# Kernel optimization log

Measured on AMD Instinct MI355X. Metric: run time of the kernel, lower is better.

Reference implementation:

```python
import jax, jax.numpy as jnp
import numpy as np

D_MODEL = 1024
NUM_HEADS = 16
D_K = D_MODEL // NUM_HEADS
SIM_THRESH = 0.7


def setup_inputs() -> dict:
    key = jax.random.key(0)
    ks = jax.random.split(key, 7)
    bs, seq = 2, 2048
    scale = 1.0 / np.sqrt(D_MODEL)
    x = jax.random.normal(ks[0], (bs, seq, D_MODEL), dtype=jnp.float32)
    Wq = jax.random.normal(ks[1], (D_MODEL, D_MODEL), dtype=jnp.float32) * scale
    Wk = jax.random.normal(ks[2], (D_MODEL, D_MODEL), dtype=jnp.float32) * scale
    Wv = jax.random.normal(ks[3], (D_MODEL, D_MODEL), dtype=jnp.float32) * scale
    bq = jax.random.normal(ks[4], (D_MODEL,), dtype=jnp.float32) * scale
    bk = jax.random.normal(ks[5], (D_MODEL,), dtype=jnp.float32) * scale
    bv = jax.random.normal(ks[6], (D_MODEL,), dtype=jnp.float32) * scale
    return {"x": x, "Wq": Wq, "bq": bq, "Wk": Wk, "bk": bk, "Wv": Wv, "bv": bv}


def reference(x, Wq, bq, Wk, bk, Wv, bv):
    bs, seq, d_model = x.shape
    # dynamic structural mask: cosine similarity > 0.7, shared across heads
    norm_x = x / jnp.maximum(jnp.linalg.norm(x, axis=-1, keepdims=True), 1e-12)
    sim = jnp.einsum('bsd,btd->bst', norm_x, norm_x)          # [B,S,S]
    mask = (sim > SIM_THRESH)[:, None, :, :]                  # [B,1,S,S]

    def proj(W, b):
        y = x @ W.T + b                                        # [B,S,D]
        return y.reshape(bs, seq, NUM_HEADS, D_K).transpose(0, 2, 1, 3)  # [B,H,S,dk]

    q = proj(Wq, bq)
    k = proj(Wk, bk)
    v = proj(Wv, bv)

    scores = jnp.einsum('bhsd,bhtd->bhst', q, k) / jnp.sqrt(jnp.float32(D_K))
    scores = jnp.where(mask, scores, -jnp.inf)
    attn = jax.nn.softmax(scores, axis=-1)                     # diag always unmasked
    return jnp.einsum('bhst,bhtd->bhsd', attn, v)              # [B,H,S,dk]
```

## Files before the change

kernel.cpp:

```cpp
#include <hip/hip_runtime.h>
#include <stdint.h>
#include <math.h>

#define D_MODEL 1024
#define NUM_HEADS 16
#define D_K 64
#define SEQ 2048
#define BATCH 2
#define SIM_THRESH 0.7f

#define TS 128
#define BK 32
#define NIT (D_MODEL / BK)

#define NROWS (BATCH * SEQ)
#define VP_BLOCKS ((NROWS / TS) * (D_MODEL / TS))
#define SIM_ROWB (SEQ / TS)
#define SIM_TRI (SIM_ROWB * (SIM_ROWB + 1) / 2)
#define SIM_BLOCKS (SIM_TRI * BATCH)
#define GRID (VP_BLOCKS + SIM_BLOCKS)

#define TILE_SH (TS * BK)

typedef __attribute__((ext_vector_type(8))) short bf16x8;
typedef __attribute__((ext_vector_type(4))) float f32x4;

static __device__ __forceinline__ unsigned short f2bf(float f) {
    unsigned int u = __float_as_uint(f);
    unsigned int r = (u + 0x7FFF + ((u >> 16) & 1)) >> 16;
    return (unsigned short)r;
}
static __device__ __forceinline__ float bf2f(unsigned short u) {
    return __uint_as_float(((unsigned int)u) << 16);
}

__global__ __launch_bounds__(256) void k_prep(const float* __restrict__ x,
                                              const float* __restrict__ Wv,
                                              unsigned short* __restrict__ xn,
                                              unsigned short* __restrict__ Wvb,
                                              float* __restrict__ norms,
                                              int* __restrict__ cnt) {
    int bid = blockIdx.x, tid = threadIdx.x;
    if (bid < NROWS) {
        const float4* xr = (const float4*)(x + (size_t)bid * D_MODEL);
        float4 vv = xr[tid];
        float ss = vv.x * vv.x + vv.y * vv.y + vv.z * vv.z + vv.w * vv.w;
        for (int off = 32; off > 0; off >>= 1) ss += __shfl_down(ss, off, 64);
        __shared__ float wsum[4];
        int lane = tid & 63, wv = tid >> 6;
        if (lane == 0) wsum[wv] = ss;
        __syncthreads();
        float nrm = sqrtf(wsum[0] + wsum[1] + wsum[2] + wsum[3]);
        float inv = 1.0f / fmaxf(nrm, 1e-12f);
        ushort4 o;
        o.x = f2bf(vv.x * inv); o.y = f2bf(vv.y * inv);
        o.z = f2bf(vv.z * inv); o.w = f2bf(vv.w * inv);
        *(ushort4*)(xn + (size_t)bid * D_MODEL + tid * 4) = o;
        if (tid == 0) { norms[bid] = nrm; cnt[bid] = 0; }
    } else {
        size_t i = (size_t)(bid - NROWS) * 256 + tid;
        float4 w = ((const float4*)Wv)[i];
        ushort4 o;
        o.x = f2bf(w.x); o.y = f2bf(w.y); o.z = f2bf(w.z); o.w = f2bf(w.w);
        *(ushort4*)(Wvb + i * 4) = o;
    }
}

static __device__ __forceinline__ void stage128x32(const unsigned short* __restrict__ gsrc,
                                                   int kk, short* ldsDst, int tid) {
#pragma unroll
    for (int i = 0; i < 2; ++i) {
        int c   = i * 256 + tid;
        int row = c >> 2;
        int ch  = c & 3;
        const unsigned short* ga = gsrc + (size_t)row * D_MODEL + kk + ch * 8;
        __builtin_amdgcn_global_load_lds(
            (const __attribute__((address_space(1))) unsigned int*)ga,
            (__attribute__((address_space(3))) unsigned int*)(ldsDst + c * 8),
            16, 0, 0);
    }
}

__global__ __launch_bounds__(256) void k_main(const unsigned short* __restrict__ xn,
                                              const unsigned short* __restrict__ Wvb,
                                              const float* __restrict__ bv,
                                              const float* __restrict__ norms,
                                              int* __restrict__ cnt,
                                              float* __restrict__ out) {
    __shared__ short As[2 * TILE_SH];
    __shared__ short Bs[2 * TILE_SH];
    int bid = blockIdx.x;
    int tid = threadIdx.x;
    int lane = tid & 63, wave = tid >> 6;
    int wm = wave & 1, wn = wave >> 1;
    int lrow = lane & 15, quad = lane >> 4;

    const unsigned short* Asrc;
    const unsigned short* Bsrc;
    int rowBase, colBase;
    bool isV;
    int b = 0, bi = 0, bj = 0;
    if (bid < VP_BLOCKS) {
        isV = true;
        rowBase = (bid >> 3) * TS;
        colBase = (bid & 7) * TS;
        Asrc = xn + (size_t)rowBase * D_MODEL;
        Bsrc = Wvb + (size_t)colBase * D_MODEL;
    } else {
        isV = false;
        int sidx = bid - VP_BLOCKS;
        b = (sidx >= SIM_TRI) ? 1 : 0;
        int r = sidx - b * SIM_TRI;
        bi = 0;
        while (r >= SIM_ROWB - bi) { r -= SIM_ROWB - bi; ++bi; }
        bj = bi + r;
        rowBase = bi * TS;
        colBase = bj * TS;
        const unsigned short* base = xn + (size_t)b * SEQ * D_MODEL;
        Asrc = base + (size_t)rowBase * D_MODEL;
        Bsrc = base + (size_t)colBase * D_MODEL;
    }

    int aoff[4], boff[4];
#pragma unroll
    for (int i = 0; i < 4; ++i) {
        aoff[i] = (wm * 64 + i * 16 + lrow) * BK + quad * 8;
        boff[i] = (wn * 64 + i * 16 + lrow) * BK + quad * 8;
    }
    f32x4 acc[4][4] = {};

    stage128x32(Asrc, 0, As, tid);
    stage128x32(Bsrc, 0, Bs, tid);
    __syncthreads();
    for (int it = 0; it < NIT; ++it) {
        int cur = it & 1, nxt = cur ^ 1;
        if (it + 1 < NIT) {
            stage128x32(Asrc, (it + 1) * BK, As + nxt * TILE_SH, tid);
            stage128x32(Bsrc, (it + 1) * BK, Bs + nxt * TILE_SH, tid);
        }
        const short* Ac = As + cur * TILE_SH;
        const short* Bc = Bs + cur * TILE_SH;
        bf16x8 av[4], bvv[4];
#pragma unroll
        for (int i = 0; i < 4; ++i) av[i]  = *(const bf16x8*)(Ac + aoff[i]);
#pragma unroll
        for (int i = 0; i < 4; ++i) bvv[i] = *(const bf16x8*)(Bc + boff[i]);
#pragma unroll
        for (int mt = 0; mt < 4; ++mt)
#pragma unroll
            for (int nt = 0; nt < 4; ++nt)
                acc[mt][nt] = __builtin_amdgcn_mfma_f32_16x16x32_bf16(av[mt], bvv[nt], acc[mt][nt], 0, 0, 0);
        __syncthreads();
    }

    if (isV) {
#pragma unroll
        for (int nt = 0; nt < 4; ++nt) {
            int n = colBase + wn * 64 + nt * 16 + lrow;
            float bn = bv[n];
            int h = n >> 6, j = n & 63;
#pragma unroll
            for (int mt = 0; mt < 4; ++mt) {
#pragma unroll
                for (int r = 0; r < 4; ++r) {
                    int m = rowBase + wm * 64 + mt * 16 + quad * 4 + r;
                    float val = acc[mt][nt][r] * norms[m] + bn;
                    int bb = m >> 11, s = m & (SEQ - 1);
                    out[(((size_t)(bb * NUM_HEADS + h)) * SEQ + s) * D_K + j] = val;
                }
            }
        }
    } else {
        int* cb = cnt + b * SEQ;
        bool diag = (bi == bj);
#pragma unroll
        for (int nt = 0; nt < 4; ++nt) {
            int n = colBase + wn * 64 + nt * 16 + lrow;
#pragma unroll
            for (int mt = 0; mt < 4; ++mt) {
#pragma unroll
                for (int r = 0; r < 4; ++r) {
                    int m = rowBase + wm * 64 + mt * 16 + quad * 4 + r;
                    if (acc[mt][nt][r] > SIM_THRESH) {
                        atomicAdd(&cb[m], 1);
                        if (!diag) atomicAdd(&cb[n], 1);
                    }
                }
            }
        }
    }
}

__global__ __launch_bounds__(256) void k_fix(
    const float* __restrict__ x,
    const float* __restrict__ Wq, const float* __restrict__ bq,
    const float* __restrict__ Wk, const float* __restrict__ bk,
    const float* __restrict__ Wv, const float* __restrict__ bv,
    const unsigned short* __restrict__ xn,
    const int* __restrict__ cnt,
    float* __restrict__ out)
{
    int tid = threadIdx.x;
    int rowBase = blockIdx.x * 256;

    __shared__ int list[256];
    __shared__ int nlist;
    if (tid == 0) nlist = 0;
    __syncthreads();
    int grow = rowBase + tid;
    if (cnt[grow] != 1) { int p = atomicAdd(&nlist, 1); list[p] = grow; }
    __syncthreads();
    int nfix = nlist;
    if (nfix == 0) return;

    __shared__ uint8_t mrow[SEQ];
    __shared__ float q_row[D_MODEL];
    __shared__ float k_row[D_MODEL];
    __shared__ float v_row[D_MODEL];
    __shared__ float accO[D_MODEL];
    __shared__ float m_h[NUM_HEADS], l_h[NUM_HEADS], alpha_h[NUM_HEADS], p_h[NUM_HEADS];

    for (int li = 0; li < nfix; ++li) {
        int row = list[li];
        int b = row >> 11, s = row & (SEQ - 1);

        const unsigned short* xs = xn + (size_t)row * D_MODEL;
        for (int t = tid; t < SEQ; t += 256) {
            const unsigned short* xt = xn + ((size_t)b * SEQ + t) * D_MODEL;
            float d = 0.f;
            for (int k = 0; k < D_MODEL; ++k) d += bf2f(xs[k]) * bf2f(xt[k]);
            mrow[t] = (d > SIM_THRESH) ? 1 : 0;
        }

        const float* xrow = x + (size_t)row * D_MODEL;
        for (int c = tid; c < D_MODEL; c += 256) {
            const float* w = Wq + (size_t)c * D_MODEL;
            float acc = bq[c];
            for (int d = 0; d < D_MODEL; ++d) acc += xrow[d] * w[d];
            q_row[c] = acc;
            accO[c] = 0.f;
        }
        if (tid < NUM_HEADS) { m_h[tid] = -INFINITY; l_h[tid] = 0.f; }
        __syncthreads();

        for (int t = 0; t < SEQ; ++t) {
            if (!mrow[t]) continue;
            const float* xt = x + ((size_t)b * SEQ + t) * D_MODEL;
            for (int c = tid; c < D_MODEL; c += 256) {
                const float* wk = Wk + (size_t)c * D_MODEL;
                const float* wv = Wv + (size_t)c * D_MODEL;
                float ak = bk[c], av = bv[c];
                for (int d = 0; d < D_MODEL; ++d) {
                    float xv = xt[d];
                    ak += xv * wk[d];
                    av += xv * wv[d];
                }
                k_row[c] = ak;
                v_row[c] = av;
            }
            __syncthreads();
            if (tid < NUM_HEADS) {
                float sc = 0.f;
                for (int j = 0; j < D_K; ++j) sc += q_row[tid * D_K + j] * k_row[tid * D_K + j];
                sc *= 0.125f;
                float mnew = fmaxf(m_h[tid], sc);
                float alpha = expf(m_h[tid] - mnew);
                float p = expf(sc - mnew);
                l_h[tid] = l_h[tid] * alpha + p;
                m_h[tid] = mnew;
                alpha_h[tid] = alpha;
                p_h[tid] = p;
            }
            __syncthreads();
            for (int c = tid; c < D_MODEL; c += 256) {
                int h = c >> 6;
                accO[c] = accO[c] * alpha_h[h] + p_h[h] * v_row[c];
            }
            __syncthreads();
        }
        for (int c = tid; c < D_MODEL; c += 256) {
            int h = c >> 6, j = c & 63;
            out[(((size_t)(b * NUM_HEADS + h)) * SEQ + s) * D_K + j] = accO[c] / l_h[h];
        }
        __syncthreads();
    }
}

extern "C" void kernel_launch(void* const* d_in, const int* in_sizes, int n_in,
                              void* d_out, int out_size, void* d_ws, size_t ws_size,
                              hipStream_t stream) {
    const float* x  = (const float*)d_in[0];
    const float* Wq = (const float*)d_in[1];
    const float* bq = (const float*)d_in[2];
    const float* Wk = (const float*)d_in[3];
    const float* bk = (const float*)d_in[4];
    const float* Wv = (const float*)d_in[5];
    const float* bv = (const float*)d_in[6];
    float* out = (float*)d_out;

    unsigned short* xn  = (unsigned short*)d_ws;
    unsigned short* Wvb = xn + (size_t)NROWS * D_MODEL;
    float* norms = (float*)(Wvb + (size_t)D_MODEL * D_MODEL);
    int* cnt     = (int*)(norms + NROWS);

    k_prep<<<NROWS + D_MODEL * D_MODEL / 1024, 256, 0, stream>>>(x, Wv, xn, Wvb, norms, cnt);

    k_main<<<GRID, 256, 0, stream>>>(xn, Wvb, bv, norms, cnt, out);

    k_fix<<<NROWS / 256, 256, 0, stream>>>(x, Wq, bq, Wk, bk, Wv, bv, xn, cnt, out);
}
```

Measured before the change: 134.8 us.

## Replace LDS-staged 128-tile GEMM with single-wave 64-tile register-streamed GEMM

The fused V-projection and similarity kernel drops LDS staging and block-wide barriers. It now runs one-wave blocks over 64x64 tiles, loading bf16 fragments straight from global memory into registers with two-stage register double buffering. The block index is swizzled across eight groups to spread tiles over the device. This removes __syncthreads and LDS round-trips and raises the block count. The cost is halved operand reuse per tile, so more traffic to L2 and global memory, plus uncoalesced row-strided 16-byte loads.

```diff
diff --git a/kernel.cpp b/kernel.cpp
--- a/kernel.cpp
+++ b/kernel.cpp
@@ -9,7 +9,7 @@
 #define BATCH 2
 #define SIM_THRESH 0.7f
 
-#define TS 128
+#define TS 64
 #define BK 32
 #define NIT (D_MODEL / BK)
 
@@ -19,8 +19,6 @@
 #define SIM_TRI (SIM_ROWB * (SIM_ROWB + 1) / 2)
 #define SIM_BLOCKS (SIM_TRI * BATCH)
 #define GRID (VP_BLOCKS + SIM_BLOCKS)
-
-#define TILE_SH (TS * BK)
 
 typedef __attribute__((ext_vector_type(8))) short bf16x8;
 typedef __attribute__((ext_vector_type(4))) float f32x4;
@@ -66,33 +64,15 @@
     }
 }
 
-static __device__ __forceinline__ void stage128x32(const unsigned short* __restrict__ gsrc,
-                                                   int kk, short* ldsDst, int tid) {
-#pragma unroll
-    for (int i = 0; i < 2; ++i) {
-        int c   = i * 256 + tid;
-        int row = c >> 2;
-        int ch  = c & 3;
-        const unsigned short* ga = gsrc + (size_t)row * D_MODEL + kk + ch * 8;
-        __builtin_amdgcn_global_load_lds(
-            (const __attribute__((address_space(1))) unsigned int*)ga,
-            (__attribute__((address_space(3))) unsigned int*)(ldsDst + c * 8),
-            16, 0, 0);
-    }
-}
-
-__global__ __launch_bounds__(256) void k_main(const unsigned short* __restrict__ xn,
-                                              const unsigned short* __restrict__ Wvb,
-                                              const float* __restrict__ bv,
-                                              const float* __restrict__ norms,
-                                              int* __restrict__ cnt,
-                                              float* __restrict__ out) {
-    __shared__ short As[2 * TILE_SH];
-    __shared__ short Bs[2 * TILE_SH];
-    int bid = blockIdx.x;
-    int tid = threadIdx.x;
-    int lane = tid & 63, wave = tid >> 6;
-    int wm = wave & 1, wn = wave >> 1;
+__global__ __launch_bounds__(64) void k_main(const unsigned short* __restrict__ xn,
+                                             const unsigned short* __restrict__ Wvb,
+                                             const float* __restrict__ bv,
+                                             const float* __restrict__ norms,
+                                             int* __restrict__ cnt,
+                                             float* __restrict__ out) {
+    int bid0 = blockIdx.x;
+    int bid = (bid0 & 7) * (GRID / 8) + (bid0 >> 3);
+    int lane = threadIdx.x;
     int lrow = lane & 15, quad = lane >> 4;
 
     const unsigned short* Asrc;
@@ -102,8 +82,8 @@
     int b = 0, bi = 0, bj = 0;
     if (bid < VP_BLOCKS) {
         isV = true;
-        rowBase = (bid >> 3) * TS;
-        colBase = (bid & 7) * TS;
+        rowBase = (bid >> 4) * TS;
+        colBase = (bid & 15) * TS;
         Asrc = xn + (size_t)rowBase * D_MODEL;
         Bsrc = Wvb + (size_t)colBase * D_MODEL;
     } else {
@@ -121,49 +101,58 @@
         Bsrc = base + (size_t)colBase * D_MODEL;
     }
 
-    int aoff[4], boff[4];
+    const unsigned short* ap[4];
+    const unsigned short* bp[4];
 #pragma unroll
     for (int i = 0; i < 4; ++i) {
-        aoff[i] = (wm * 64 + i * 16 + lrow) * BK + quad * 8;
-        boff[i] = (wn * 64 + i * 16 + lrow) * BK + quad * 8;
-    }
+        ap[i] = Asrc + (size_t)(i * 16 + lrow) * D_MODEL + quad * 8;
+        bp[i] = Bsrc + (size_t)(i * 16 + lrow) * D_MODEL + quad * 8;
+    }
+
     f32x4 acc[4][4] = {};
-
-    stage128x32(Asrc, 0, As, tid);
-    stage128x32(Bsrc, 0, Bs, tid);
-    __syncthreads();
-    for (int it = 0; it < NIT; ++it) {
-        int cur = it & 1, nxt = cur ^ 1;
-        if (it + 1 < NIT) {
-            stage128x32(Asrc, (it + 1) * BK, As + nxt * TILE_SH, tid);
-            stage128x32(Bsrc, (it + 1) * BK, Bs + nxt * TILE_SH, tid);
-        }
-        const short* Ac = As + cur * TILE_SH;
-        const short* Bc = Bs + cur * TILE_SH;
-        bf16x8 av[4], bvv[4];
-#pragma unroll
-        for (int i = 0; i < 4; ++i) av[i]  = *(const bf16x8*)(Ac + aoff[i]);
-#pragma unroll
-        for (int i = 0; i < 4; ++i) bvv[i] = *(const bf16x8*)(Bc + boff[i]);
+    bf16x8 a0[4], b0[4], a1[4], b1[4];
+
+#pragma unroll
+    for (int i = 0; i < 4; ++i) {
+        a0[i] = *(const bf16x8*)(ap[i]);
+        b0[i] = *(const bf16x8*)(bp[i]);
+    }
+    for (int it = 0; it < NIT; it += 2) {
+#pragma unroll
+        for (int i = 0; i < 4; ++i) {
+            a1[i] = *(const bf16x8*)(ap[i] + (it + 1) * BK);
+            b1[i] = *(const bf16x8*)(bp[i] + (it + 1) * BK);
+        }
 #pragma unroll
         for (int mt = 0; mt < 4; ++mt)
 #pragma unroll
             for (int nt = 0; nt < 4; ++nt)
-                acc[mt][nt] = __builtin_amdgcn_mfma_f32_16x16x32_bf16(av[mt], bvv[nt], acc[mt][nt], 0, 0, 0);
-        __syncthreads();
+                acc[mt][nt] = __builtin_amdgcn_mfma_f32_16x16x32_bf16(a0[mt], b0[nt], acc[mt][nt], 0, 0, 0);
+        if (it + 2 < NIT) {
+#pragma unroll
+            for (int i = 0; i < 4; ++i) {
+                a0[i] = *(const bf16x8*)(ap[i] + (it + 2) * BK);
+                b0[i] = *(const bf16x8*)(bp[i] + (it + 2) * BK);
+            }
+        }
+#pragma unroll
+        for (int mt = 0; mt < 4; ++mt)
+#pragma unroll
+            for (int nt = 0; nt < 4; ++nt)
+                acc[mt][nt] = __builtin_amdgcn_mfma_f32_16x16x32_bf16(a1[mt], b1[nt], acc[mt][nt], 0, 0, 0);
     }
 
     if (isV) {
 #pragma unroll
         for (int nt = 0; nt < 4; ++nt) {
-            int n = colBase + wn * 64 + nt * 16 + lrow;
+            int n = colBase + nt * 16 + lrow;
             float bn = bv[n];
             int h = n >> 6, j = n & 63;
 #pragma unroll
             for (int mt = 0; mt < 4; ++mt) {
 #pragma unroll
                 for (int r = 0; r < 4; ++r) {
-                    int m = rowBase + wm * 64 + mt * 16 + quad * 4 + r;
+                    int m = rowBase + mt * 16 + quad * 4 + r;
                     float val = acc[mt][nt][r] * norms[m] + bn;
                     int bb = m >> 11, s = m & (SEQ - 1);
                     out[(((size_t)(bb * NUM_HEADS + h)) * SEQ + s) * D_K + j] = val;
@@ -175,12 +164,12 @@
         bool diag = (bi == bj);
 #pragma unroll
         for (int nt = 0; nt < 4; ++nt) {
-            int n = colBase + wn * 64 + nt * 16 + lrow;
+            int n = colBase + nt * 16 + lrow;
 #pragma unroll
             for (int mt = 0; mt < 4; ++mt) {
 #pragma unroll
                 for (int r = 0; r < 4; ++r) {
-                    int m = rowBase + wm * 64 + mt * 16 + quad * 4 + r;
+                    int m = rowBase + mt * 16 + quad * 4 + r;
                     if (acc[mt][nt][r] > SIM_THRESH) {
                         atomicAdd(&cb[m], 1);
                         if (!diag) atomicAdd(&cb[n], 1);
@@ -305,7 +294,7 @@
 
     k_prep<<<NROWS + D_MODEL * D_MODEL / 1024, 256, 0, stream>>>(x, Wv, xn, Wvb, norms, cnt);
 
-    k_main<<<GRID, 256, 0, stream>>>(xn, Wvb, bv, norms, cnt, out);
+    k_main<<<GRID, 64, 0, stream>>>(xn, Wvb, bv, norms, cnt, out);
 
     k_fix<<<NROWS / 256, 256, 0, stream>>>(x, Wq, bq, Wk, bk, Wv, bv, xn, cnt, out);
 }
```

After: 158.5 us. 17.6% more time.

## Compute similarity mask with int8 MFMA and remap blocks per XCD

Applied to the files above, without the earlier changes.

Quantizes the normalized rows to int8 (scaled by 127) in the prep kernel and computes the cosine-similarity tiles with i32 16x16x64 int8 MFMA against an integer threshold. This halves the bytes loaded per similarity tile and doubles MFMA throughput compared with bf16. Blocks are also remapped so each XCD gets a contiguous share of V-projection and similarity tiles, and the kernel asks for 3 blocks per CU through launch bounds. The int8 rounding may flip mask decisions for pairs near the 0.7 threshold, and the extra int8 buffer costs some prep bandwidth.

```diff
diff --git a/kernel.cpp b/kernel.cpp
--- a/kernel.cpp
+++ b/kernel.cpp
@@ -8,10 +8,13 @@
 #define SEQ 2048
 #define BATCH 2
 #define SIM_THRESH 0.7f
+#define ITHRESH 11290
 
 #define TS 128
-#define BK 32
-#define NIT (D_MODEL / BK)
+#define BKV 32
+#define NITV (D_MODEL / BKV)
+#define BKS 64
+#define NITS (D_MODEL / BKS)
 
 #define NROWS (BATCH * SEQ)
 #define VP_BLOCKS ((NROWS / TS) * (D_MODEL / TS))
@@ -19,11 +22,14 @@
 #define SIM_TRI (SIM_ROWB * (SIM_ROWB + 1) / 2)
 #define SIM_BLOCKS (SIM_TRI * BATCH)
 #define GRID (VP_BLOCKS + SIM_BLOCKS)
-
-#define TILE_SH (TS * BK)
+#define VP_PER_XCD (VP_BLOCKS / 8)
+#define SIM_PER_XCD (SIM_BLOCKS / 8)
+
+#define TILE_B 8192
 
 typedef __attribute__((ext_vector_type(8))) short bf16x8;
 typedef __attribute__((ext_vector_type(4))) float f32x4;
+typedef __attribute__((ext_vector_type(4))) int i32x4;
 
 static __device__ __forceinline__ unsigned short f2bf(float f) {
     unsigned int u = __float_as_uint(f);
@@ -38,6 +44,7 @@
                                               const float* __restrict__ Wv,
                                               unsigned short* __restrict__ xn,
                                               unsigned short* __restrict__ Wvb,
+                                              char* __restrict__ xq,
                                               float* __restrict__ norms,
                                               int* __restrict__ cnt) {
     int bid = blockIdx.x, tid = threadIdx.x;
@@ -52,10 +59,16 @@
         __syncthreads();
         float nrm = sqrtf(wsum[0] + wsum[1] + wsum[2] + wsum[3]);
         float inv = 1.0f / fmaxf(nrm, 1e-12f);
+        float n0 = vv.x * inv, n1 = vv.y * inv, n2 = vv.z * inv, n3 = vv.w * inv;
         ushort4 o;
-        o.x = f2bf(vv.x * inv); o.y = f2bf(vv.y * inv);
-        o.z = f2bf(vv.z * inv); o.w = f2bf(vv.w * inv);
+        o.x = f2bf(n0); o.y = f2bf(n1); o.z = f2bf(n2); o.w = f2bf(n3);
         *(ushort4*)(xn + (size_t)bid * D_MODEL + tid * 4) = o;
+        char4 q;
+        q.x = (char)__float2int_rn(n0 * 127.f);
+        q.y = (char)__float2int_rn(n1 * 127.f);
+        q.z = (char)__float2int_rn(n2 * 127.f);
+        q.w = (char)__float2int_rn(n3 * 127.f);
+        *(char4*)(xq + (size_t)bid * D_MODEL + tid * 4) = q;
         if (tid == 0) { norms[bid] = nrm; cnt[bid] = 0; }
     } else {
         size_t i = (size_t)(bid - NROWS) * 256 + tid;
@@ -66,94 +79,78 @@
     }
 }
 
-static __device__ __forceinline__ void stage128x32(const unsigned short* __restrict__ gsrc,
-                                                   int kk, short* ldsDst, int tid) {
+static __device__ __forceinline__ void stage8k(const char* __restrict__ gsrc,
+                                               int rowStrideB, int kByte,
+                                               char* ldsDst, int tid) {
 #pragma unroll
     for (int i = 0; i < 2; ++i) {
         int c   = i * 256 + tid;
         int row = c >> 2;
         int ch  = c & 3;
-        const unsigned short* ga = gsrc + (size_t)row * D_MODEL + kk + ch * 8;
+        const char* ga = gsrc + (size_t)row * rowStrideB + kByte + ch * 16;
         __builtin_amdgcn_global_load_lds(
             (const __attribute__((address_space(1))) unsigned int*)ga,
-            (__attribute__((address_space(3))) unsigned int*)(ldsDst + c * 8),
+            (__attribute__((address_space(3))) unsigned int*)(ldsDst + c * 16),
             16, 0, 0);
     }
 }
 
-__global__ __launch_bounds__(256) void k_main(const unsigned short* __restrict__ xn,
-                                              const unsigned short* __restrict__ Wvb,
-                                              const float* __restrict__ bv,
-                                              const float* __restrict__ norms,
-                                              int* __restrict__ cnt,
-                                              float* __restrict__ out) {
-    __shared__ short As[2 * TILE_SH];
-    __shared__ short Bs[2 * TILE_SH];
-    int bid = blockIdx.x;
+__global__ __launch_bounds__(256, 3) void k_main(const unsigned short* __restrict__ xn,
+                                                 const unsigned short* __restrict__ Wvb,
+                                                 const char* __restrict__ xq,
+                                                 const float* __restrict__ bv,
+                                                 const float* __restrict__ norms,
+                                                 int* __restrict__ cnt,
+                                                 float* __restrict__ out) {
+    __shared__ char As[2 * TILE_B];
+    __shared__ char Bs[2 * TILE_B];
+    int bid0 = blockIdx.x;
+    int xcd = bid0 & 7, l = bid0 >> 3;
     int tid = threadIdx.x;
     int lane = tid & 63, wave = tid >> 6;
     int wm = wave & 1, wn = wave >> 1;
     int lrow = lane & 15, quad = lane >> 4;
 
-    const unsigned short* Asrc;
-    const unsigned short* Bsrc;
-    int rowBase, colBase;
-    bool isV;
-    int b = 0, bi = 0, bj = 0;
-    if (bid < VP_BLOCKS) {
-        isV = true;
-        rowBase = (bid >> 3) * TS;
-        colBase = (bid & 7) * TS;
-        Asrc = xn + (size_t)rowBase * D_MODEL;
-        Bsrc = Wvb + (size_t)colBase * D_MODEL;
-    } else {
-        isV = false;
-        int sidx = bid - VP_BLOCKS;
-        b = (sidx >= SIM_TRI) ? 1 : 0;
-        int r = sidx - b * SIM_TRI;
-        bi = 0;
-        while (r >= SIM_ROWB - bi) { r -= SIM_ROWB - bi; ++bi; }
-        bj = bi + r;
-        rowBase = bi * TS;
-        colBase = bj * TS;
-        const unsigned short* base = xn + (size_t)b * SEQ * D_MODEL;
-        Asrc = base + (size_t)rowBase * D_MODEL;
-        Bsrc = base + (size_t)colBase * D_MODEL;
-    }
-
-    int aoff[4], boff[4];
+    bool isV = (l < VP_PER_XCD);
+
+    int aoffB[4], boffB[4];
 #pragma unroll
     for (int i = 0; i < 4; ++i) {
-        aoff[i] = (wm * 64 + i * 16 + lrow) * BK + quad * 8;
-        boff[i] = (wn * 64 + i * 16 + lrow) * BK + quad * 8;
-    }
-    f32x4 acc[4][4] = {};
-
-    stage128x32(Asrc, 0, As, tid);
-    stage128x32(Bsrc, 0, Bs, tid);
-    __syncthreads();
-    for (int it = 0; it < NIT; ++it) {
-        int cur = it & 1, nxt = cur ^ 1;
-        if (it + 1 < NIT) {
-            stage128x32(Asrc, (it + 1) * BK, As + nxt * TILE_SH, tid);
-            stage128x32(Bsrc, (it + 1) * BK, Bs + nxt * TILE_SH, tid);
-        }
-        const short* Ac = As + cur * TILE_SH;
-        const short* Bc = Bs + cur * TILE_SH;
-        bf16x8 av[4], bvv[4];
-#pragma unroll
-        for (int i = 0; i < 4; ++i) av[i]  = *(const bf16x8*)(Ac + aoff[i]);
-#pragma unroll
-        for (int i = 0; i < 4; ++i) bvv[i] = *(const bf16x8*)(Bc + boff[i]);
-#pragma unroll
-        for (int mt = 0; mt < 4; ++mt)
-#pragma unroll
-            for (int nt = 0; nt < 4; ++nt)
-                acc[mt][nt] = __builtin_amdgcn_mfma_f32_16x16x32_bf16(av[mt], bvv[nt], acc[mt][nt], 0, 0, 0);
-        __syncthreads();
+        aoffB[i] = (wm * 64 + i * 16 + lrow) * 64 + quad * 16;
+        boffB[i] = (wn * 64 + i * 16 + lrow) * 64 + quad * 16;
     }
 
     if (isV) {
+        int bid = xcd * VP_PER_XCD + l;
+        int rowBase = (bid >> 3) * TS;
+        int colBase = (bid & 7) * TS;
+        const char* Asrc = (const char*)(xn + (size_t)rowBase * D_MODEL);
+        const char* Bsrc = (const char*)(Wvb + (size_t)colBase * D_MODEL);
+
+        f32x4 acc[4][4] = {};
+        stage8k(Asrc, D_MODEL * 2, 0, As, tid);
+        stage8k(Bsrc, D_MODEL * 2, 0, Bs, tid);
+        __syncthreads();
+        for (int it = 0; it < NITV; ++it) {
+            int cur = it & 1, nxt = cur ^ 1;
+            if (it + 1 < NITV) {
+                stage8k(Asrc, D_MODEL * 2, (it + 1) * 64, As + nxt * TILE_B, tid);
+                stage8k(Bsrc, D_MODEL * 2, (it + 1) * 64, Bs + nxt * TILE_B, tid);
+            }
+            const char* Ac = As + cur * TILE_B;
+            const char* Bc = Bs + cur * TILE_B;
+            bf16x8 av[4], bw[4];
+#pragma unroll
+            for (int i = 0; i < 4; ++i) av[i] = *(const bf16x8*)(Ac + aoffB[i]);
+#pragma unroll
+            for (int i = 0; i < 4; ++i) bw[i] = *(const bf16x8*)(Bc + boffB[i]);
+#pragma unroll
+            for (int mt = 0; mt < 4; ++mt)
+#pragma unroll
+                for (int nt = 0; nt < 4; ++nt)
+                    acc[mt][nt] = __builtin_amdgcn_mfma_f32_16x16x32_bf16(av[mt], bw[nt], acc[mt][nt], 0, 0, 0);
+            __syncthreads();
+        }
 #pragma unroll
         for (int nt = 0; nt < 4; ++nt) {
             int n = colBase + wn * 64 + nt * 16 + lrow;
@@ -171,6 +168,42 @@
             }
         }
     } else {
+        int sidx = xcd * SIM_PER_XCD + (l - VP_PER_XCD);
+        int b = (sidx >= SIM_TRI) ? 1 : 0;
+        int r0 = sidx - b * SIM_TRI;
+        int bi = 0;
+        while (r0 >= SIM_ROWB - bi) { r0 -= SIM_ROWB - bi; ++bi; }
+        int bj = bi + r0;
+        int rowBase = bi * TS;
+        int colBase = bj * TS;
+        const char* base = xq + (size_t)b * SEQ * D_MODEL;
+        const char* Asrc = base + (size_t)rowBase * D_MODEL;
+        const char* Bsrc = base + (size_t)colBase * D_MODEL;
+
+        i32x4 acc[4][4] = {};
+        stage8k(Asrc, D_MODEL, 0, As, tid);
+        stage8k(Bsrc, D_MODEL, 0, Bs, tid);
+        __syncthreads();
+        for (int it = 0; it < NITS; ++it) {
+            int cur = it & 1, nxt = cur ^ 1;
+            if (it + 1 < NITS) {
+                stage8k(Asrc, D_MODEL, (it + 1) * 64, As + nxt * TILE_B, tid);
+                stage8k(Bsrc, D_MODEL, (it + 1) * 64, Bs + nxt * TILE_B, tid);
+            }
+            const char* Ac = As + cur * TILE_B;
+            const char* Bc = Bs + cur * TILE_B;
+            i32x4 av[4], bw[4];
+#pragma unroll
+            for (int i = 0; i < 4; ++i) av[i] = *(const i32x4*)(Ac + aoffB[i]);
+#pragma unroll
+            for (int i = 0; i < 4; ++i) bw[i] = *(const i32x4*)(Bc + boffB[i]);
+#pragma unroll
+            for (int mt = 0; mt < 4; ++mt)
+#pragma unroll
+                for (int nt = 0; nt < 4; ++nt)
+                    acc[mt][nt] = __builtin_amdgcn_mfma_i32_16x16x64_i8(av[mt], bw[nt], acc[mt][nt], 0, 0, 0);
+            __syncthreads();
+        }
         int* cb = cnt + b * SEQ;
         bool diag = (bi == bj);
 #pragma unroll
@@ -181,7 +214,7 @@
 #pragma unroll
                 for (int r = 0; r < 4; ++r) {
                     int m = rowBase + wm * 64 + mt * 16 + quad * 4 + r;
-                    if (acc[mt][nt][r] > SIM_THRESH) {
+                    if (acc[mt][nt][r] > ITHRESH) {
                         atomicAdd(&cb[m], 1);
                         if (!diag) atomicAdd(&cb[n], 1);
                     }
@@ -300,12 +333,13 @@
 
     unsigned short* xn  = (unsigned short*)d_ws;
     unsigned short* Wvb = xn + (size_t)NROWS * D_MODEL;
-    float* norms = (float*)(Wvb + (size_t)D_MODEL * D_MODEL);
+    char* xq     = (char*)(Wvb + (size_t)D_MODEL * D_MODEL);
+    float* norms = (float*)(xq + (size_t)NROWS * D_MODEL);
     int* cnt     = (int*)(norms + NROWS);
 
-    k_prep<<<NROWS + D_MODEL * D_MODEL / 1024, 256, 0, stream>>>(x, Wv, xn, Wvb, norms, cnt);
-
-    k_main<<<GRID, 256, 0, stream>>>(xn, Wvb, bv, norms, cnt, out);
+    k_prep<<<NROWS + D_MODEL * D_MODEL / 1024, 256, 0, stream>>>(x, Wv, xn, Wvb, xq, norms, cnt);
+
+    k_main<<<GRID, 256, 0, stream>>>(xn, Wvb, xq, bv, norms, cnt, out);
 
     k_fix<<<NROWS / 256, 256, 0, stream>>>(x, Wq, bq, Wk, bk, Wv, bv, xn, cnt, out);
 }
```

Result: faster. 109.4 us (-18.9%).
